# Kernel tuning notes

Hardware: AMD Instinct MI355X
Metric: run time of the kernel (lower is better)

The kernel has to match this reference:

```python
import jax, jax.numpy as jnp
import numpy as np

N_NODES, N_EDGES, FEA_DIM, H_DIM, N_LAYER, N_GRAPHS, LABEL_DIM = 50000, 600000, 128, 256, 3, 256, 2


def setup_inputs() -> dict:
    key = jax.random.key(0)
    ks = jax.random.split(key, 8)
    x = jax.random.normal(ks[0], (N_NODES, FEA_DIM), jnp.float32)
    edge_index = jax.random.randint(ks[1], (2, N_EDGES), 0, N_NODES, dtype=jnp.int64)
    batch = jnp.sort(jax.random.randint(ks[2], (N_NODES,), 0, N_GRAPHS, dtype=jnp.int64))
    Wg = jax.random.normal(ks[3], (N_LAYER, FEA_DIM, FEA_DIM), jnp.float32) / np.sqrt(FEA_DIM)
    bg = jnp.zeros((N_LAYER, FEA_DIM), jnp.float32)
    w1 = jax.random.normal(ks[4], (FEA_DIM, H_DIM), jnp.float32) / np.sqrt(FEA_DIM)
    b1 = jnp.zeros((H_DIM,), jnp.float32)
    w2 = jax.random.normal(ks[5], (H_DIM, LABEL_DIM), jnp.float32) / np.sqrt(H_DIM)
    b2 = jnp.zeros((LABEL_DIM,), jnp.float32)
    return dict(x=x, Wg=Wg, bg=bg, w1=w1, b1=b1, w2=w2, b2=b2,
                edge_index=edge_index, batch=batch)


def reference(x, Wg, bg, w1, b1, w2, b2, edge_index, batch):
    N = x.shape[0]
    # --- GCN normalization with self-loops (PyG GCNConv default) ---
    loop = jnp.arange(N, dtype=edge_index.dtype)
    src = jnp.concatenate([edge_index[0], loop])  # [E+N]
    dst = jnp.concatenate([edge_index[1], loop])
    deg = jax.ops.segment_sum(jnp.ones_like(src, x.dtype), dst, num_segments=N)
    dinv = jnp.where(deg > 0, jax.lax.rsqrt(jnp.maximum(deg, 1.0)), 0.0)
    norm = dinv[src] * dinv[dst]  # [E+N]
    # --- stacked GCNConv + ReLU ---
    for l in range(Wg.shape[0]):
        h = x @ Wg[l]                              # [N, D] linear transform
        msg = h[src] * norm[:, None]               # gather + edge scale
        x = jax.ops.segment_sum(msg, dst, num_segments=N) + bg[l]  # scatter-add
        x = jax.nn.relu(x)
    # --- global mean pool over graphs ---
    sums = jax.ops.segment_sum(x, batch, num_segments=N_GRAPHS)
    counts = jax.ops.segment_sum(jnp.ones((N, 1), x.dtype), batch, num_segments=N_GRAPHS)
    pooled = sums / jnp.maximum(counts, 1.0)       # [G, D]
    # --- MLP head ---
    h = jax.nn.relu(pooled @ w1 + b1)
    return h @ w2 + b2                             # [G, label_dim]
```

## Files before the change

kernel.cpp:

```cpp
#include <hip/hip_runtime.h>
#include <hip/hip_bf16.h>

#define N_NODES 50000
#define N_EDGES 600000
#define FEA_DIM 128
#define H_DIM 256
#define N_LAYER 3
#define N_GRAPHS 256
#define LABEL_DIM 2

#define SCAN_NB ((N_NODES + 255) / 256)
#define GEMM_NB ((N_NODES + 63) / 64)
#define COUNT_NB ((N_EDGES + 255) / 256)


__device__ __forceinline__ void gemm_body(const float* __restrict__ X, const float* __restrict__ W,
                                          float* __restrict__ H, int M, int tile) {
    __shared__ float a_s[32][68];
    __shared__ float b_s[32][128];
    const int tid = threadIdx.x;
    const int row_g = tid >> 4;
    const int col_g = tid & 15;
    const int row_base = tile * 64;
    float acc[4][8] = {};

    for (int kt = 0; kt < 4; ++kt) {
        const int k0 = kt * 32;
#pragma unroll
        for (int j = 0; j < 2; ++j) {
            int id = tid + j * 256;
            int m = id >> 3;
            int kq = (id & 7) << 2;
            float4 v = make_float4(0.f, 0.f, 0.f, 0.f);
            int gr = row_base + m;
            if (gr < M) v = *(const float4*)(X + gr * 128 + k0 + kq);
            a_s[kq + 0][m] = v.x; a_s[kq + 1][m] = v.y;
            a_s[kq + 2][m] = v.z; a_s[kq + 3][m] = v.w;
        }
#pragma unroll
        for (int j = 0; j < 4; ++j) {
            int id = tid + j * 256;
            int k = id >> 5;
            int n = (id & 31) << 2;
            *(float4*)(&b_s[k][n]) = *(const float4*)(W + (k0 + k) * 128 + n);
        }
        __syncthreads();
#pragma unroll 8
        for (int k = 0; k < 32; ++k) {
            float4 a0 = *(const float4*)(&a_s[k][row_g * 4]);
            float4 b0 = *(const float4*)(&b_s[k][col_g * 4]);
            float4 b1 = *(const float4*)(&b_s[k][64 + col_g * 4]);
            float av[4] = {a0.x, a0.y, a0.z, a0.w};
            float bv[8] = {b0.x, b0.y, b0.z, b0.w, b1.x, b1.y, b1.z, b1.w};
#pragma unroll
            for (int i = 0; i < 4; ++i)
#pragma unroll
                for (int jj = 0; jj < 8; ++jj) acc[i][jj] += av[i] * bv[jj];
        }
        __syncthreads();
    }
#pragma unroll
    for (int i = 0; i < 4; ++i) {
        int gr = row_base + row_g * 4 + i;
        if (gr < M) {
            float4 o0 = {acc[i][0], acc[i][1], acc[i][2], acc[i][3]};
            float4 o1 = {acc[i][4], acc[i][5], acc[i][6], acc[i][7]};
            *(float4*)(H + gr * 128 + col_g * 4) = o0;
            *(float4*)(H + gr * 128 + 64 + col_g * 4) = o1;
        }
    }
}

__global__ __launch_bounds__(256) void k_gemm(const float* __restrict__ X, const float* __restrict__ W,
                                              float* __restrict__ H, int M) {
    gemm_body(X, W, H, M, blockIdx.x);
}

__global__ __launch_bounds__(256) void k_gemm0_count(const float* __restrict__ X, const float* __restrict__ W,
                                                     float* __restrict__ H,
                                                     const int* __restrict__ dst, int* __restrict__ counts) {
    if (blockIdx.x < GEMM_NB) {
        gemm_body(X, W, H, N_NODES, blockIdx.x);
    } else {
        int e = (blockIdx.x - GEMM_NB) * 256 + threadIdx.x;
        if (e < N_EDGES) atomicAdd(&counts[dst[e]], 1);
    }
}


__global__ __launch_bounds__(256) void k_partial(const int* __restrict__ counts, int* __restrict__ partial) {
    int g = blockIdx.x * 256 + threadIdx.x;
    int v = (g < N_NODES) ? counts[g] : 0;
#pragma unroll
    for (int off = 32; off > 0; off >>= 1) v += __shfl_down(v, off);
    __shared__ int ws[4];
    int lane = threadIdx.x & 63, wid = threadIdx.x >> 6;
    if (lane == 0) ws[wid] = v;
    __syncthreads();
    if (threadIdx.x == 0) partial[blockIdx.x] = ws[0] + ws[1] + ws[2] + ws[3];
}

__global__ __launch_bounds__(256) void k_rowptr(const int* __restrict__ counts, const int* __restrict__ partial,
                                                int* __restrict__ row_ptr, float* __restrict__ dinv,
                                                int* __restrict__ cursor) {
    __shared__ int sp[256];
    __shared__ int s[256];
    int tid = threadIdx.x;
    sp[tid] = (tid < SCAN_NB) ? partial[tid] : 0;
    __syncthreads();
#pragma unroll
    for (int off = 1; off < 256; off <<= 1) {
        int t = (tid >= off) ? sp[tid - off] : 0;
        __syncthreads();
        sp[tid] += t;
        __syncthreads();
    }
    int block_off = (blockIdx.x == 0) ? 0 : sp[blockIdx.x - 1];

    int g = blockIdx.x * 256 + tid;
    int c = (g < N_NODES) ? counts[g] : 0;
    s[tid] = c;
    __syncthreads();
#pragma unroll
    for (int off = 1; off < 256; off <<= 1) {
        int t = (tid >= off) ? s[tid - off] : 0;
        __syncthreads();
        s[tid] += t;
        __syncthreads();
    }
    if (g < N_NODES) {
        row_ptr[g] = block_off + s[tid] - c;
        dinv[g] = rsqrtf((float)c + 1.0f);
        cursor[g] = 0;
    }
    if (blockIdx.x == 0 && tid == 0) row_ptr[N_NODES] = sp[SCAN_NB - 1];
}

__global__ __launch_bounds__(256) void k_fill(const int* __restrict__ src, const int* __restrict__ dst,
                                              const int* __restrict__ row_ptr, int* __restrict__ cursor,
                                              int* __restrict__ col) {
    int e = blockIdx.x * 256 + threadIdx.x;
    if (e >= N_EDGES) return;
    int s = src[e], d = dst[e];
    int p = row_ptr[d] + atomicAdd(&cursor[d], 1);
    col[p] = s;
}


__global__ __launch_bounds__(256) void k_agg(const float* __restrict__ H, const float* __restrict__ bgl,
                                             const int* __restrict__ row_ptr, const int* __restrict__ col,
                                             const float* __restrict__ dinv,
                                             float* __restrict__ Xo) {
    const int i = (blockIdx.x * 256 + threadIdx.x) >> 5;
    if (i >= N_NODES) return;
    const int fl = threadIdx.x & 31;
    const float4* H4 = (const float4*)H;
    const float di = dinv[i];
    float4 h = H4[(size_t)i * 32 + fl];
    const float wself = di * di;
    float4 acc = make_float4(h.x * wself, h.y * wself, h.z * wself, h.w * wself);
    const int p0 = row_ptr[i], p1 = row_ptr[i + 1];
    for (int base = p0; base < p1; base += 32) {
        int m = p1 - base; if (m > 32) m = 32;
        int sc = 0; float wc = 0.f;
        if (fl < m) { sc = col[base + fl]; wc = dinv[sc] * di; }
        float4 hb0[8], hb1[8]; float wb0[8], wb1[8];
        int cnt0 = (m < 8) ? m : 8;
#pragma unroll
        for (int t = 0; t < 8; ++t) {
            if (t < cnt0) {
                int s = __shfl(sc, t, 32);
                wb0[t] = __shfl(wc, t, 32);
                hb0[t] = H4[(size_t)s * 32 + fl];
            }
        }
        for (int j = 8; j < m; j += 8) {
            int cnt1 = m - j; if (cnt1 > 8) cnt1 = 8;
#pragma unroll
            for (int t = 0; t < 8; ++t) {
                if (t < cnt1) {
                    int s = __shfl(sc, j + t, 32);
                    wb1[t] = __shfl(wc, j + t, 32);
                    hb1[t] = H4[(size_t)s * 32 + fl];
                }
            }
#pragma unroll
            for (int t = 0; t < 8; ++t) {
                if (t < cnt0) {
                    acc.x += hb0[t].x * wb0[t];
                    acc.y += hb0[t].y * wb0[t];
                    acc.z += hb0[t].z * wb0[t];
                    acc.w += hb0[t].w * wb0[t];
                }
            }
#pragma unroll
            for (int t = 0; t < 8; ++t) { hb0[t] = hb1[t]; wb0[t] = wb1[t]; }
            cnt0 = cnt1;
        }
#pragma unroll
        for (int t = 0; t < 8; ++t) {
            if (t < cnt0) {
                acc.x += hb0[t].x * wb0[t];
                acc.y += hb0[t].y * wb0[t];
                acc.z += hb0[t].z * wb0[t];
                acc.w += hb0[t].w * wb0[t];
            }
        }
    }
    float4 b = ((const float4*)bgl)[fl];
    float4 o;
    o.x = fmaxf(acc.x + b.x, 0.f);
    o.y = fmaxf(acc.y + b.y, 0.f);
    o.z = fmaxf(acc.z + b.z, 0.f);
    o.w = fmaxf(acc.w + b.w, 0.f);
    ((float4*)Xo)[(size_t)i * 32 + fl] = o;
}


__global__ __launch_bounds__(256) void k_poolmlp(const float* __restrict__ X, const int* __restrict__ batch,
                                                 const float* __restrict__ w1, const float* __restrict__ b1,
                                                 const float* __restrict__ w2, const float* __restrict__ b2,
                                                 float* __restrict__ out) {
    __shared__ int s_lo, s_hi;
    __shared__ float red[256];
    __shared__ float xs[128];
    __shared__ float hs[256];
    int g = blockIdx.x, tid = threadIdx.x;
    if (tid == 0) {
        int lo = 0, hi = N_NODES;
        while (lo < hi) { int mid = (lo + hi) >> 1; if (batch[mid] < g) lo = mid + 1; else hi = mid; }
        s_lo = lo;
        int lo2 = lo, hi2 = N_NODES;
        while (lo2 < hi2) { int mid = (lo2 + hi2) >> 1; if (batch[mid] < g + 1) lo2 = mid + 1; else hi2 = mid; }
        s_hi = lo2;
    }
    __syncthreads();
    int lo = s_lo, hi = s_hi;
    int f = tid & 127, half = tid >> 7;
    float acc = 0.f;
    for (int r = lo + half; r < hi; r += 2) acc += X[r * 128 + f];
    red[tid] = acc;
    __syncthreads();
    if (tid < 128) {
        int cnt = hi - lo;
        xs[tid] = (red[tid] + red[tid + 128]) / (float)(cnt > 0 ? cnt : 1);
    }
    __syncthreads();
    float a1 = b1[tid];
#pragma unroll 8
    for (int k = 0; k < 128; ++k) a1 += xs[k] * w1[k * H_DIM + tid];
    hs[tid] = fmaxf(a1, 0.f);
    __syncthreads();
    int j = tid >> 7, t2 = tid & 127;
    float p = hs[t2] * w2[t2 * LABEL_DIM + j] + hs[t2 + 128] * w2[(t2 + 128) * LABEL_DIM + j];
    red[tid] = p;
    __syncthreads();
    for (int s2 = 64; s2 > 0; s2 >>= 1) {
        if (t2 < s2) red[tid] += red[tid + s2];
        __syncthreads();
    }
    if (t2 == 0) out[g * LABEL_DIM + j] = red[tid] + b2[j];
}


extern "C" void kernel_launch(void* const* d_in, const int* in_sizes, int n_in,
                              void* d_out, int out_size, void* d_ws, size_t ws_size,
                              hipStream_t stream) {
    const float* x   = (const float*)d_in[0];
    const float* Wg  = (const float*)d_in[1];
    const float* bg  = (const float*)d_in[2];
    const float* w1  = (const float*)d_in[3];
    const float* b1  = (const float*)d_in[4];
    const float* w2  = (const float*)d_in[5];
    const float* b2  = (const float*)d_in[6];
    const int* eidx  = (const int*)d_in[7];
    const int* batch = (const int*)d_in[8];
    float* out = (float*)d_out;

    const int* src = eidx;
    const int* dst = eidx + N_EDGES;

    char* ws = (char*)d_ws;
    size_t off = 0;
    float* A = (float*)(ws + off); off += (size_t)N_NODES * FEA_DIM * 4;
    float* B = (float*)(ws + off); off += (size_t)N_NODES * FEA_DIM * 4;
    int*   col = (int*)(ws + off); off += (size_t)N_EDGES * 4;
    int*   row_ptr = (int*)(ws + off); off += 200704;
    int*   cursor  = (int*)(ws + off); off += 200704;
    int*   counts  = (int*)(ws + off); off += 200704;
    float* dinv    = (float*)(ws + off); off += 200704;
    int*   partial = (int*)(ws + off); off += 4096;

    hipMemsetAsync(counts, 0, 200704, stream);
    k_gemm0_count<<<GEMM_NB + COUNT_NB, 256, 0, stream>>>(x, Wg, B, dst, counts);
    k_partial<<<SCAN_NB, 256, 0, stream>>>(counts, partial);
    k_rowptr<<<SCAN_NB, 256, 0, stream>>>(counts, partial, row_ptr, dinv, cursor);
    k_fill<<<COUNT_NB, 256, 0, stream>>>(src, dst, row_ptr, cursor, col);

    k_agg<<<(N_NODES + 7) / 8, 256, 0, stream>>>(B, bg + 0 * FEA_DIM, row_ptr, col, dinv, A);
    for (int l = 1; l < N_LAYER; ++l) {
        k_gemm<<<GEMM_NB, 256, 0, stream>>>(A, Wg + (size_t)l * FEA_DIM * FEA_DIM, B, N_NODES);
        k_agg<<<(N_NODES + 7) / 8, 256, 0, stream>>>(B, bg + (size_t)l * FEA_DIM, row_ptr, col, dinv, A);
    }
    k_poolmlp<<<N_GRAPHS, 256, 0, stream>>>(A, batch, w1, b1, w2, b2, out);
}
```

Measured before the change: 389.0 us.

## Fuse GCN aggregation with the next layer's GEMM in one kernel

Adds a k_agg_gemm kernel. Each block aggregates 64 nodes into shared memory (transposed), then multiplies that tile by the next layer's weight matrix and writes the transformed features directly. This removes the full write and re-read of the intermediate node-feature matrix between aggregation and GEMM, and drops two kernel launches. In exchange, the gather-heavy aggregation runs with far fewer blocks and a larger shared-memory footprint (about 51KB), which may reduce occupancy and the latency hiding the sparse gathers depend on. The transposed shared-memory stores may also cause bank conflicts.

```diff
diff --git a/kernel.cpp b/kernel.cpp
--- a/kernel.cpp
+++ b/kernel.cpp
@@ -71,11 +71,6 @@
     }
 }
 
-__global__ __launch_bounds__(256) void k_gemm(const float* __restrict__ X, const float* __restrict__ W,
-                                              float* __restrict__ H, int M) {
-    gemm_body(X, W, H, M, blockIdx.x);
-}
-
 __global__ __launch_bounds__(256) void k_gemm0_count(const float* __restrict__ X, const float* __restrict__ W,
                                                      float* __restrict__ H,
                                                      const int* __restrict__ dst, int* __restrict__ counts) {
@@ -88,73 +83,9 @@
 }
 
 
-__global__ __launch_bounds__(256) void k_partial(const int* __restrict__ counts, int* __restrict__ partial) {
-    int g = blockIdx.x * 256 + threadIdx.x;
-    int v = (g < N_NODES) ? counts[g] : 0;
-#pragma unroll
-    for (int off = 32; off > 0; off >>= 1) v += __shfl_down(v, off);
-    __shared__ int ws[4];
-    int lane = threadIdx.x & 63, wid = threadIdx.x >> 6;
-    if (lane == 0) ws[wid] = v;
-    __syncthreads();
-    if (threadIdx.x == 0) partial[blockIdx.x] = ws[0] + ws[1] + ws[2] + ws[3];
-}
-
-__global__ __launch_bounds__(256) void k_rowptr(const int* __restrict__ counts, const int* __restrict__ partial,
-                                                int* __restrict__ row_ptr, float* __restrict__ dinv,
-                                                int* __restrict__ cursor) {
-    __shared__ int sp[256];
-    __shared__ int s[256];
-    int tid = threadIdx.x;
-    sp[tid] = (tid < SCAN_NB) ? partial[tid] : 0;
-    __syncthreads();
-#pragma unroll
-    for (int off = 1; off < 256; off <<= 1) {
-        int t = (tid >= off) ? sp[tid - off] : 0;
-        __syncthreads();
-        sp[tid] += t;
-        __syncthreads();
-    }
-    int block_off = (blockIdx.x == 0) ? 0 : sp[blockIdx.x - 1];
-
-    int g = blockIdx.x * 256 + tid;
-    int c = (g < N_NODES) ? counts[g] : 0;
-    s[tid] = c;
-    __syncthreads();
-#pragma unroll
-    for (int off = 1; off < 256; off <<= 1) {
-        int t = (tid >= off) ? s[tid - off] : 0;
-        __syncthreads();
-        s[tid] += t;
-        __syncthreads();
-    }
-    if (g < N_NODES) {
-        row_ptr[g] = block_off + s[tid] - c;
-        dinv[g] = rsqrtf((float)c + 1.0f);
-        cursor[g] = 0;
-    }
-    if (blockIdx.x == 0 && tid == 0) row_ptr[N_NODES] = sp[SCAN_NB - 1];
-}
-
-__global__ __launch_bounds__(256) void k_fill(const int* __restrict__ src, const int* __restrict__ dst,
-                                              const int* __restrict__ row_ptr, int* __restrict__ cursor,
-                                              int* __restrict__ col) {
-    int e = blockIdx.x * 256 + threadIdx.x;
-    if (e >= N_EDGES) return;
-    int s = src[e], d = dst[e];
-    int p = row_ptr[d] + atomicAdd(&cursor[d], 1);
-    col[p] = s;
-}
-
-
-__global__ __launch_bounds__(256) void k_agg(const float* __restrict__ H, const float* __restrict__ bgl,
-                                             const int* __restrict__ row_ptr, const int* __restrict__ col,
-                                             const float* __restrict__ dinv,
-                                             float* __restrict__ Xo) {
-    const int i = (blockIdx.x * 256 + threadIdx.x) >> 5;
-    if (i >= N_NODES) return;
-    const int fl = threadIdx.x & 31;
-    const float4* H4 = (const float4*)H;
+__device__ __forceinline__ float4 agg_node(const float4* __restrict__ H4, const float4* __restrict__ bgl4,
+                                           const int* __restrict__ row_ptr, const int* __restrict__ col,
+                                           const float* __restrict__ dinv, int i, int fl) {
     const float di = dinv[i];
     float4 h = H4[(size_t)i * 32 + fl];
     const float wself = di * di;
@@ -207,13 +138,149 @@
             }
         }
     }
-    float4 b = ((const float4*)bgl)[fl];
+    float4 b = bgl4[fl];
     float4 o;
     o.x = fmaxf(acc.x + b.x, 0.f);
     o.y = fmaxf(acc.y + b.y, 0.f);
     o.z = fmaxf(acc.z + b.z, 0.f);
     o.w = fmaxf(acc.w + b.w, 0.f);
+    return o;
+}
+
+
+__global__ __launch_bounds__(256) void k_agg_gemm(const float* __restrict__ H, const float* __restrict__ bgl,
+                                                  const int* __restrict__ row_ptr, const int* __restrict__ col,
+                                                  const float* __restrict__ dinv,
+                                                  const float* __restrict__ W, float* __restrict__ Hout) {
+    __shared__ float a_s[128][68];
+    __shared__ float b_s[32][128];
+    const int tid = threadIdx.x;
+    const int tile = blockIdx.x;
+    const int hw = tid >> 5;
+    const int fl = tid & 31;
+    const float4* H4 = (const float4*)H;
+    const float4* bgl4 = (const float4*)bgl;
+
+    for (int it = 0; it < 8; ++it) {
+        const int m = it * 8 + hw;
+        const int i = tile * 64 + m;
+        float4 o = make_float4(0.f, 0.f, 0.f, 0.f);
+        if (i < N_NODES) o = agg_node(H4, bgl4, row_ptr, col, dinv, i, fl);
+        a_s[4 * fl + 0][m] = o.x;
+        a_s[4 * fl + 1][m] = o.y;
+        a_s[4 * fl + 2][m] = o.z;
+        a_s[4 * fl + 3][m] = o.w;
+    }
+
+    const int row_g = tid >> 4;
+    const int col_g = tid & 15;
+    const int row_base = tile * 64;
+    float acc[4][8] = {};
+    for (int kt = 0; kt < 4; ++kt) {
+        const int k0 = kt * 32;
+#pragma unroll
+        for (int j = 0; j < 4; ++j) {
+            int id = tid + j * 256;
+            int k = id >> 5;
+            int n = (id & 31) << 2;
+            *(float4*)(&b_s[k][n]) = *(const float4*)(W + (k0 + k) * 128 + n);
+        }
+        __syncthreads();
+#pragma unroll 8
+        for (int k = 0; k < 32; ++k) {
+            float4 a0 = *(const float4*)(&a_s[k0 + k][row_g * 4]);
+            float4 b0 = *(const float4*)(&b_s[k][col_g * 4]);
+            float4 b1 = *(const float4*)(&b_s[k][64 + col_g * 4]);
+            float av[4] = {a0.x, a0.y, a0.z, a0.w};
+            float bv[8] = {b0.x, b0.y, b0.z, b0.w, b1.x, b1.y, b1.z, b1.w};
+#pragma unroll
+            for (int i = 0; i < 4; ++i)
+#pragma unroll
+                for (int jj = 0; jj < 8; ++jj) acc[i][jj] += av[i] * bv[jj];
+        }
+        __syncthreads();
+    }
+#pragma unroll
+    for (int i = 0; i < 4; ++i) {
+        int gr = row_base + row_g * 4 + i;
+        if (gr < N_NODES) {
+            float4 o0 = {acc[i][0], acc[i][1], acc[i][2], acc[i][3]};
+            float4 o1 = {acc[i][4], acc[i][5], acc[i][6], acc[i][7]};
+            *(float4*)(Hout + gr * 128 + col_g * 4) = o0;
+            *(float4*)(Hout + gr * 128 + 64 + col_g * 4) = o1;
+        }
+    }
+}
+
+
+__global__ __launch_bounds__(256) void k_agg(const float* __restrict__ H, const float* __restrict__ bgl,
+                                             const int* __restrict__ row_ptr, const int* __restrict__ col,
+                                             const float* __restrict__ dinv,
+                                             float* __restrict__ Xo) {
+    const int i = (blockIdx.x * 256 + threadIdx.x) >> 5;
+    if (i >= N_NODES) return;
+    const int fl = threadIdx.x & 31;
+    float4 o = agg_node((const float4*)H, (const float4*)bgl, row_ptr, col, dinv, i, fl);
     ((float4*)Xo)[(size_t)i * 32 + fl] = o;
+}
+
+
+__global__ __launch_bounds__(256) void k_partial(const int* __restrict__ counts, int* __restrict__ partial) {
+    int g = blockIdx.x * 256 + threadIdx.x;
+    int v = (g < N_NODES) ? counts[g] : 0;
+#pragma unroll
+    for (int off = 32; off > 0; off >>= 1) v += __shfl_down(v, off);
+    __shared__ int ws[4];
+    int lane = threadIdx.x & 63, wid = threadIdx.x >> 6;
+    if (lane == 0) ws[wid] = v;
+    __syncthreads();
+    if (threadIdx.x == 0) partial[blockIdx.x] = ws[0] + ws[1] + ws[2] + ws[3];
+}
+
+__global__ __launch_bounds__(256) void k_rowptr(const int* __restrict__ counts, const int* __restrict__ partial,
+                                                int* __restrict__ row_ptr, float* __restrict__ dinv,
+                                                int* __restrict__ cursor) {
+    __shared__ int sp[256];
+    __shared__ int s[256];
+    int tid = threadIdx.x;
+    sp[tid] = (tid < SCAN_NB) ? partial[tid] : 0;
+    __syncthreads();
+#pragma unroll
+    for (int off = 1; off < 256; off <<= 1) {
+        int t = (tid >= off) ? sp[tid - off] : 0;
+        __syncthreads();
+        sp[tid] += t;
+        __syncthreads();
+    }
+    int block_off = (blockIdx.x == 0) ? 0 : sp[blockIdx.x - 1];
+
+    int g = blockIdx.x * 256 + tid;
+    int c = (g < N_NODES) ? counts[g] : 0;
+    s[tid] = c;
+    __syncthreads();
+#pragma unroll
+    for (int off = 1; off < 256; off <<= 1) {
+        int t = (tid >= off) ? s[tid - off] : 0;
+        __syncthreads();
+        s[tid] += t;
+        __syncthreads();
+    }
+    if (g < N_NODES) {
+        row_ptr[g] = block_off + s[tid] - c;
+        dinv[g] = rsqrtf((float)c + 1.0f);
+        cursor[g] = 0;
+    }
+    if (blockIdx.x == 0 && tid == 0) row_ptr[N_NODES] = sp[SCAN_NB - 1];
+}
+
+__global__ __launch_bounds__(256) void k_fill(const int* __restrict__ src, const int* __restrict__ dst,
+                                              const int* __restrict__ row_ptr, int* __restrict__ cursor,
+                                              int* __restrict__ col) {
+    int e = blockIdx.x * 256 + threadIdx.x;
+    if (e >= N_EDGES) return;
+    int s = src[e], d = dst[e];
+    int p = row_ptr[d] + atomicAdd(&cursor[d], 1);
+    col[p] = s;
 }
 
 
@@ -297,10 +364,10 @@
     k_rowptr<<<SCAN_NB, 256, 0, stream>>>(counts, partial, row_ptr, dinv, cursor);
     k_fill<<<COUNT_NB, 256, 0, stream>>>(src, dst, row_ptr, cursor, col);
 
-    k_agg<<<(N_NODES + 7) / 8, 256, 0, stream>>>(B, bg + 0 * FEA_DIM, row_ptr, col, dinv, A);
-    for (int l = 1; l < N_LAYER; ++l) {
-        k_gemm<<<GEMM_NB, 256, 0, stream>>>(A, Wg + (size_t)l * FEA_DIM * FEA_DIM, B, N_NODES);
-        k_agg<<<(N_NODES + 7) / 8, 256, 0, stream>>>(B, bg + (size_t)l * FEA_DIM, row_ptr, col, dinv, A);
-    }
+    k_agg_gemm<<<GEMM_NB, 256, 0, stream>>>(B, bg + 0 * FEA_DIM, row_ptr, col, dinv,
+                                            Wg + 1 * FEA_DIM * FEA_DIM, A);
+    k_agg_gemm<<<GEMM_NB, 256, 0, stream>>>(A, bg + 1 * FEA_DIM, row_ptr, col, dinv,
+                                            Wg + 2 * FEA_DIM * FEA_DIM, B);
+    k_agg<<<(N_NODES + 7) / 8, 256, 0, stream>>>(B, bg + 2 * FEA_DIM, row_ptr, col, dinv, A);
     k_poolmlp<<<N_GRAPHS, 256, 0, stream>>>(A, batch, w1, b1, w2, b2, out);
 }
```

New measurement: 414.6 us. 6.6% more time.
